# Kernel optimization log

Hardware: AMD Instinct MI355X
Metric: run time of the kernel (lower is better)

## Reference

```python
import jax, jax.numpy as jnp
from jax import lax
import numpy as np


def _gaussian_kernels(k, sigma):
    # spatial Gaussian kernel per sample; sigma: (B,) -> (B, k, k), normalized
    coords = jnp.arange(k) - k // 2
    grid = (coords[None, :] ** 2 + coords[:, None] ** 2).astype(jnp.float32)
    ker = jnp.exp(-grid[None, :, :] / (2.0 * sigma[:, None, None] ** 2))
    return ker / ker.sum(axis=(1, 2), keepdims=True)


def setup_inputs() -> dict:
    key = jax.random.key(0)
    kx, kp = jax.random.split(key)
    x = jax.random.normal(kx, (8, 64, 384, 384), dtype=jnp.float32)
    params = jax.random.normal(kp, (8, 2), dtype=jnp.float32)
    return {"x": x, "params": params}


def reference(x, params):
    B, C, H, W = x.shape
    # torch: params[:,0].long() truncates toward zero, then sigmoid, then int()
    k_int = jnp.trunc(params[:, 0])
    k_sel = jnp.floor(5.0 + 5.0 * jax.nn.sigmoid(k_int)).astype(jnp.int32)  # (B,) in {5..9}
    sigma = 0.5 + 4.5 * jax.nn.sigmoid(params[:, 1])                        # (B,)

    out = jnp.zeros_like(x)
    # small fixed set of possible kernel sizes (structurally distinct convs)
    for k in range(5, 10):
        ker = _gaussian_kernels(k, sigma)  # (B, k, k)
        pad = k // 2

        def conv_one(xi, ki, pad=pad):
            # depthwise conv with the same (k,k) kernel for every channel:
            # treat channels as batch, single-in single-out kernel.
            y = lax.conv_general_dilated(xi[:, None], ki[None, None],
                                         window_strides=(1, 1),
                                         padding=[(pad, pad), (pad, pad)])
            return y[:, 0]

        y = jax.vmap(conv_one)(x, ker)  # (B, C, H', W'); H'=H+1 when k even
        if k % 2 == 0:
            # F.interpolate bilinear align_corners=False == half-pixel, no antialias
            y = jax.image.resize(y, (B, C, H, W), method='bilinear', antialias=False)
        out = jnp.where((k_sel == k)[:, None, None, None], y, out)
    return out
```

## Files before the change

### kernel.cpp

```cpp
#include <hip/hip_runtime.h>
#include <math.h>

#define B_  8
#define C_  64
#define H_  384
#define W_  384

#define TX   64
#define TY   32
#define HALO 4
#define SW   (TX + 2*HALO)
#define SH   (TY + 2*HALO)
#define SWP  76
#define TXP  68

#define NTX     (W_ / TX)
#define NTY     (H_ / TY)
#define NTILES  (NTX * NTY)
#define NBLK    (NTILES * C_ * B_)

typedef float f2v __attribute__((ext_vector_type(2)));

template<int K>
__device__ __forceinline__ void process_tile(
    float (*sIn)[SWP], float (*sTmp)[TXP],
    float* __restrict__ op, int tx0, int ty0, float sigma, int tid)
{
    constexpr int  PAD  = K / 2;
    constexpr bool EVEN = ((K & 1) == 0);

    float g[K];
    {
        const float inv2s2 = 1.0f / (2.0f * sigma * sigma);
        float S = 0.0f;
        #pragma unroll
        for (int i = 0; i < K; ++i) {
            float d = (float)(i - PAD);
            g[i] = expf(-d * d * inv2s2);
            S += g[i];
        }
        const float invS = 1.0f / S;
        #pragma unroll
        for (int i = 0; i < K; ++i) g[i] *= invS;
    }

    for (int li = tid; li < SH * 8; li += 256) {
        const int r  = li >> 3;
        const int g8 = (li & 7) * 8;
        float V[16];
        #pragma unroll
        for (int i = 0; i < 16; ++i) V[i] = sIn[r][g8 + i];
        float vals[8];
        #pragma unroll
        for (int j = 0; j < 8; ++j) {
            float a0 = 0.0f;
            #pragma unroll
            for (int t = 0; t < K; ++t) a0 += g[t] * V[j + 4 - PAD + t];
            float val = a0;
            if (EVEN) {
                float a1 = 0.0f;
                #pragma unroll
                for (int t = 0; t < K; ++t) a1 += g[t] * V[j + 5 - PAD + t];
                const float fw = ((float)(tx0 + g8 + j) + 0.5f) * (1.0f / (float)W_);
                val = a0 + fw * (a1 - a0);
            }
            vals[j] = val;
        }
        *reinterpret_cast<float4*>(&sTmp[r][g8])     = make_float4(vals[0], vals[1], vals[2], vals[3]);
        *reinterpret_cast<float4*>(&sTmp[r][g8 + 4]) = make_float4(vals[4], vals[5], vals[6], vals[7]);
    }
    __syncthreads();

    {
        const int yg = tid >> 5;
        const int x2 = (tid & 31) * 2;
        f2v U[12];
        #pragma unroll
        for (int i = 0; i < 12; ++i)
            U[i] = *reinterpret_cast<const f2v*>(&sTmp[yg * 4 + i][x2]);
        #pragma unroll
        for (int j = 0; j < 4; ++j) {
            f2v a0 = {0.0f, 0.0f};
            #pragma unroll
            for (int t = 0; t < K; ++t) a0 += g[t] * U[j + 4 - PAD + t];
            f2v val = a0;
            if (EVEN) {
                f2v a1 = {0.0f, 0.0f};
                #pragma unroll
                for (int t = 0; t < K; ++t) a1 += g[t] * U[j + 5 - PAD + t];
                const float fh = ((float)(ty0 + yg * 4 + j) + 0.5f) * (1.0f / (float)H_);
                val = a0 + fh * (a1 - a0);
            }
            __builtin_nontemporal_store(val,
                reinterpret_cast<f2v*>(&op[(size_t)(ty0 + yg * 4 + j) * W_ + (tx0 + x2)]));
        }
    }
}

__global__ __launch_bounds__(256) void gauss_blur_kernel(
    const float* __restrict__ x, const float* __restrict__ params,
    float* __restrict__ out)
{
    const int bid  = blockIdx.x;
    const int gidx = (bid & 7) * (NBLK / 8) + (bid >> 3);

    const int tile = gidx % NTILES;
    const int bc   = gidx / NTILES;
    const int c    = bc & (C_ - 1);
    const int b    = bc >> 6;

    const int tx0  = (tile % NTX) * TX;
    const int ty0  = (tile / NTX) * TY;

    const float p0 = params[2 * b + 0];
    const float p1 = params[2 * b + 1];
    const float k_int = truncf(p0);
    const float s0 = 1.0f / (1.0f + expf(-k_int));
    int k = (int)floorf(5.0f + 5.0f * s0);
    if (k < 5) k = 5;
    if (k > 9) k = 9;
    const float sigma = 0.5f + 4.5f * (1.0f / (1.0f + expf(-p1)));

    __shared__ float sIn[SH][SWP];
    __shared__ float sTmp[SH][TXP];

    const size_t plane = (size_t)(b * C_ + c) * (size_t)(H_ * W_);
    const float* xp = x + plane;
    float*       op = out + plane;
    const int tid = threadIdx.x;

    for (int li = tid; li < SH * (SW / 4); li += 256) {
        const int r  = li / (SW / 4);
        const int c4 = li - r * (SW / 4);
        const int gr = ty0 - HALO + r;
        const int gc = tx0 - HALO + c4 * 4;
        float4 v = make_float4(0.f, 0.f, 0.f, 0.f);
        if (gr >= 0 && gr < H_ && gc >= 0 && gc < W_)
            v = *reinterpret_cast<const float4*>(xp + (size_t)gr * W_ + gc);
        *reinterpret_cast<float4*>(&sIn[r][c4 * 4]) = v;
    }
    __syncthreads();

    switch (k) {
        case 5:  process_tile<5>(sIn, sTmp, op, tx0, ty0, sigma, tid); break;
        case 6:  process_tile<6>(sIn, sTmp, op, tx0, ty0, sigma, tid); break;
        case 7:  process_tile<7>(sIn, sTmp, op, tx0, ty0, sigma, tid); break;
        case 8:  process_tile<8>(sIn, sTmp, op, tx0, ty0, sigma, tid); break;
        default: process_tile<9>(sIn, sTmp, op, tx0, ty0, sigma, tid); break;
    }
}

extern "C" void kernel_launch(void* const* d_in, const int* in_sizes, int n_in,
                              void* d_out, int out_size, void* d_ws, size_t ws_size,
                              hipStream_t stream) {
    const float* x      = (const float*)d_in[0];
    const float* params = (const float*)d_in[1];
    float* out          = (float*)d_out;

    dim3 grid(NBLK, 1, 1);
    dim3 block(256, 1, 1);
    gauss_blur_kernel<<<grid, block, 0, stream>>>(x, params, out);
}
```

Before: 491.2 us.

## Stream full-width row strips through a shared-memory ring buffer with register prefetch

Replaces 64x32 tiles with full-width 192-row strips per block, streaming four rows at a time. Each lane loads six columns into registers and gets its horizontal halo from neighbouring lanes by wave shuffles. Horizontal results go into a 16-row shared ring that the vertical pass reads. This removes the horizontal and vertical halo reloads of the tiled scheme and prefetches the next row into registers. In exchange it needs a barrier per 4-row step, uses fewer and longer blocks, and leaves a quarter of the threads idle in the vertical pass.

```diff
diff --git a/kernel.cpp b/kernel.cpp
--- a/kernel.cpp
+++ b/kernel.cpp
@@ -6,28 +6,26 @@
 #define H_  384
 #define W_  384
 
-#define TX   64
-#define TY   32
-#define HALO 4
-#define SW   (TX + 2*HALO)
-#define SH   (TY + 2*HALO)
-#define SWP  76
-#define TXP  68
-
-#define NTX     (W_ / TX)
-#define NTY     (H_ / TY)
-#define NTILES  (NTX * NTY)
-#define NBLK    (NTILES * C_ * B_)
+#define RY      192
+#define NSTR    (H_ / RY)
+#define NPLANE  (B_ * C_)
+#define NBLK    (NPLANE * NSTR)
+#define RINGW   392
+#define NCHUNK  ((RY + 8) / 4)
 
 typedef float f2v __attribute__((ext_vector_type(2)));
 
 template<int K>
-__device__ __forceinline__ void process_tile(
-    float (*sIn)[SWP], float (*sTmp)[TXP],
-    float* __restrict__ op, int tx0, int ty0, float sigma, int tid)
+__device__ __forceinline__ void run_strip(
+    float (*ring)[RINGW],
+    const float* __restrict__ xp, float* __restrict__ op,
+    int sy0, float sigma, int tid)
 {
     constexpr int  PAD  = K / 2;
     constexpr bool EVEN = ((K & 1) == 0);
+    const int wv = tid >> 6;
+    const int ln = tid & 63;
+    const int x0 = 6 * ln;
 
     float g[K];
     {
@@ -44,56 +42,94 @@
         for (int i = 0; i < K; ++i) g[i] *= invS;
     }
 
-    for (int li = tid; li < SH * 8; li += 256) {
-        const int r  = li >> 3;
-        const int g8 = (li & 7) * 8;
-        float V[16];
+    auto loadrow = [&](float (&d)[6], int j) {
+        const int r = sy0 - 4 + 4 * j + wv;
+        if (j < NCHUNK && r >= 0 && r < H_) {
+            const float* rp = xp + (size_t)r * W_ + x0;
+            f2v a = *reinterpret_cast<const f2v*>(rp);
+            f2v b = *reinterpret_cast<const f2v*>(rp + 2);
+            f2v c = *reinterpret_cast<const f2v*>(rp + 4);
+            d[0] = a.x; d[1] = a.y; d[2] = b.x;
+            d[3] = b.y; d[4] = c.x; d[5] = c.y;
+        } else {
+            #pragma unroll
+            for (int i = 0; i < 6; ++i) d[i] = 0.f;
+        }
+    };
+
+    auto step = [&](int j, float (&cur)[6], float (&nxt)[6]) {
+        loadrow(nxt, j + 1);
+
+        float w[14];
         #pragma unroll
-        for (int i = 0; i < 16; ++i) V[i] = sIn[r][g8 + i];
-        float vals[8];
+        for (int i = 0; i < 6; ++i) w[4 + i] = cur[i];
         #pragma unroll
-        for (int j = 0; j < 8; ++j) {
-            float a0 = 0.0f;
+        for (int i = 0; i < 4; ++i) {
+            float t = __shfl_up(cur[2 + i], 1, 64);
+            w[i] = (ln == 0) ? 0.f : t;
+        }
+        #pragma unroll
+        for (int i = 0; i < 4; ++i) {
+            float t = __shfl_down(cur[i], 1, 64);
+            w[10 + i] = (ln == 63) ? 0.f : t;
+        }
+
+        float hv[6];
+        #pragma unroll
+        for (int cc = 0; cc < 6; ++cc) {
+            float a0 = 0.f;
             #pragma unroll
-            for (int t = 0; t < K; ++t) a0 += g[t] * V[j + 4 - PAD + t];
+            for (int t = 0; t < K; ++t) a0 += g[t] * w[cc + 4 - PAD + t];
             float val = a0;
             if (EVEN) {
-                float a1 = 0.0f;
+                float a1 = 0.f;
                 #pragma unroll
-                for (int t = 0; t < K; ++t) a1 += g[t] * V[j + 5 - PAD + t];
-                const float fw = ((float)(tx0 + g8 + j) + 0.5f) * (1.0f / (float)W_);
+                for (int t = 0; t < K; ++t) a1 += g[t] * w[cc + 5 - PAD + t];
+                const float fw = ((float)(x0 + cc) + 0.5f) * (1.0f / (float)W_);
                 val = a0 + fw * (a1 - a0);
             }
-            vals[j] = val;
+            hv[cc] = val;
         }
-        *reinterpret_cast<float4*>(&sTmp[r][g8])     = make_float4(vals[0], vals[1], vals[2], vals[3]);
-        *reinterpret_cast<float4*>(&sTmp[r][g8 + 4]) = make_float4(vals[4], vals[5], vals[6], vals[7]);
-    }
-    __syncthreads();
+        const int slot = (4 * j + wv) & 15;
+        f2v p0 = { hv[0], hv[1] }, p1 = { hv[2], hv[3] }, p2 = { hv[4], hv[5] };
+        *reinterpret_cast<f2v*>(&ring[slot][x0])     = p0;
+        *reinterpret_cast<f2v*>(&ring[slot][x0 + 2]) = p1;
+        *reinterpret_cast<f2v*>(&ring[slot][x0 + 4]) = p2;
 
-    {
-        const int yg = tid >> 5;
-        const int x2 = (tid & 31) * 2;
-        f2v U[12];
-        #pragma unroll
-        for (int i = 0; i < 12; ++i)
-            U[i] = *reinterpret_cast<const f2v*>(&sTmp[yg * 4 + i][x2]);
-        #pragma unroll
-        for (int j = 0; j < 4; ++j) {
-            f2v a0 = {0.0f, 0.0f};
+        __syncthreads();
+
+        if (j >= 2 && tid < 192) {
+            const int m  = j - 2;
+            const int xx = 2 * tid;
+            f2v U[12];
             #pragma unroll
-            for (int t = 0; t < K; ++t) a0 += g[t] * U[j + 4 - PAD + t];
-            f2v val = a0;
-            if (EVEN) {
-                f2v a1 = {0.0f, 0.0f};
+            for (int i = 0; i < 12; ++i)
+                U[i] = *reinterpret_cast<const f2v*>(&ring[(4 * m + i) & 15][xx]);
+            #pragma unroll
+            for (int jj = 0; jj < 4; ++jj) {
+                f2v a0 = { 0.f, 0.f };
                 #pragma unroll
-                for (int t = 0; t < K; ++t) a1 += g[t] * U[j + 5 - PAD + t];
-                const float fh = ((float)(ty0 + yg * 4 + j) + 0.5f) * (1.0f / (float)H_);
-                val = a0 + fh * (a1 - a0);
+                for (int t = 0; t < K; ++t) a0 += g[t] * U[jj + 4 - PAD + t];
+                f2v val = a0;
+                const int y = sy0 + 4 * m + jj;
+                if (EVEN) {
+                    f2v a1 = { 0.f, 0.f };
+                    #pragma unroll
+                    for (int t = 0; t < K; ++t) a1 += g[t] * U[jj + 5 - PAD + t];
+                    const float fh = ((float)y + 0.5f) * (1.0f / (float)H_);
+                    val = a0 + fh * (a1 - a0);
+                }
+                __builtin_nontemporal_store(val,
+                    reinterpret_cast<f2v*>(&op[(size_t)y * W_ + xx]));
             }
-            __builtin_nontemporal_store(val,
-                reinterpret_cast<f2v*>(&op[(size_t)(ty0 + yg * 4 + j) * W_ + (tx0 + x2)]));
         }
+    };
+
+    float bufA[6], bufB[6];
+    loadrow(bufA, 0);
+    for (int jj = 0; jj < NCHUNK / 2; ++jj) {
+        step(2 * jj,     bufA, bufB);
+        step(2 * jj + 1, bufB, bufA);
     }
 }
 
@@ -101,16 +137,13 @@
     const float* __restrict__ x, const float* __restrict__ params,
     float* __restrict__ out)
 {
-    const int bid  = blockIdx.x;
-    const int gidx = (bid & 7) * (NBLK / 8) + (bid >> 3);
-
-    const int tile = gidx % NTILES;
-    const int bc   = gidx / NTILES;
-    const int c    = bc & (C_ - 1);
-    const int b    = bc >> 6;
-
-    const int tx0  = (tile % NTX) * TX;
-    const int ty0  = (tile / NTX) * TY;
+    const int bid   = blockIdx.x;
+    const int gidx  = (bid & 7) * (NBLK / 8) + (bid >> 3);
+    const int strip = gidx & (NSTR - 1);
+    const int p     = gidx / NSTR;
+    const int c     = p & (C_ - 1);
+    const int b     = p >> 6;
+    const int sy0   = strip * RY;
 
     const float p0 = params[2 * b + 0];
     const float p1 = params[2 * b + 1];
@@ -121,32 +154,18 @@
     if (k > 9) k = 9;
     const float sigma = 0.5f + 4.5f * (1.0f / (1.0f + expf(-p1)));
 
-    __shared__ float sIn[SH][SWP];
-    __shared__ float sTmp[SH][TXP];
+    __shared__ float ring[16][RINGW];
 
     const size_t plane = (size_t)(b * C_ + c) * (size_t)(H_ * W_);
     const float* xp = x + plane;
     float*       op = out + plane;
-    const int tid = threadIdx.x;
-
-    for (int li = tid; li < SH * (SW / 4); li += 256) {
-        const int r  = li / (SW / 4);
-        const int c4 = li - r * (SW / 4);
-        const int gr = ty0 - HALO + r;
-        const int gc = tx0 - HALO + c4 * 4;
-        float4 v = make_float4(0.f, 0.f, 0.f, 0.f);
-        if (gr >= 0 && gr < H_ && gc >= 0 && gc < W_)
-            v = *reinterpret_cast<const float4*>(xp + (size_t)gr * W_ + gc);
-        *reinterpret_cast<float4*>(&sIn[r][c4 * 4]) = v;
-    }
-    __syncthreads();
 
     switch (k) {
-        case 5:  process_tile<5>(sIn, sTmp, op, tx0, ty0, sigma, tid); break;
-        case 6:  process_tile<6>(sIn, sTmp, op, tx0, ty0, sigma, tid); break;
-        case 7:  process_tile<7>(sIn, sTmp, op, tx0, ty0, sigma, tid); break;
-        case 8:  process_tile<8>(sIn, sTmp, op, tx0, ty0, sigma, tid); break;
-        default: process_tile<9>(sIn, sTmp, op, tx0, ty0, sigma, tid); break;
+        case 5:  run_strip<5>(ring, xp, op, sy0, sigma, threadIdx.x); break;
+        case 6:  run_strip<6>(ring, xp, op, sy0, sigma, threadIdx.x); break;
+        case 7:  run_strip<7>(ring, xp, op, sy0, sigma, threadIdx.x); break;
+        case 8:  run_strip<8>(ring, xp, op, sy0, sigma, threadIdx.x); break;
+        default: run_strip<9>(ring, xp, op, sy0, sigma, threadIdx.x); break;
     }
 }
 
```

Result: slower. 509.8 us (+3.8%).
